# Performance work log

Hardware: AMD Instinct MI355X
Metric: run time of the kernel (lower is better)

Reference implementation:

```python
import jax, jax.numpy as jnp
import numpy as np

B, N, S, D, K = 8, 8192, 2048, 256, 3
MLP = [256, 128]
EPS = 1e-5


def setup_inputs() -> dict:
    key = jax.random.key(0)
    ks = jax.random.split(key, 12)
    inp = {
        "xyz1": jax.random.normal(ks[0], (B, N, 3), dtype=jnp.float32),
        "xyz2": jax.random.normal(ks[1], (B, S, 3), dtype=jnp.float32),
        "points1": jax.random.normal(ks[2], (B, N, D), dtype=jnp.float32),
        "points2": jax.random.normal(ks[3], (B, S, D), dtype=jnp.float32),
        # relation conv: Conv2d(4 -> 1, kernel 1x1) == linear over last dim
        "rel_w": jax.random.normal(ks[4], (4,), dtype=jnp.float32) * 0.5,
        "rel_b": jnp.zeros((), dtype=jnp.float32),
        # mlp layer 0: Conv1d(2D -> 256, k=1) + BN
        "W0": jax.random.normal(ks[5], (MLP[0], 2 * D), dtype=jnp.float32) * (1.0 / np.sqrt(2 * D)),
        "b0": jnp.zeros((MLP[0],), dtype=jnp.float32),
        "g0": jnp.ones((MLP[0],), dtype=jnp.float32),
        "be0": jnp.zeros((MLP[0],), dtype=jnp.float32),
        # mlp layer 1: Conv1d(256 -> 128, k=1) + BN
        "W1": jax.random.normal(ks[6], (MLP[1], MLP[0]), dtype=jnp.float32) * (1.0 / np.sqrt(MLP[0])),
        "b1": jnp.zeros((MLP[1],), dtype=jnp.float32),
        "g1": jnp.ones((MLP[1],), dtype=jnp.float32),
        "be1": jnp.zeros((MLP[1],), dtype=jnp.float32),
    }
    return inp


def _gather(points, idx):
    # points: [B,S,C], idx: [B,N,K] -> [B,N,K,C]
    return jax.vmap(lambda p, i: p[i])(points, idx)


def _bn_relu(x, gamma, beta):
    # training-mode BatchNorm1d over [B,N,C]: stats over (B,N), biased var
    mean = jnp.mean(x, axis=(0, 1))
    var = jnp.var(x, axis=(0, 1))
    xn = (x - mean) * jax.lax.rsqrt(var + EPS)
    return jax.nn.relu(xn * gamma + beta)


def reference(xyz1, xyz2, points1, points2, rel_w, rel_b,
              W0, b0, g0, be0, W1, b1, g1, be1):
    # pairwise squared distances [B,N,S]
    d = (jnp.sum(xyz1 ** 2, -1)[:, :, None]
         + jnp.sum(xyz2 ** 2, -1)[:, None, :]
         - 2.0 * jnp.einsum('bnc,bmc->bnm', xyz1, xyz2))
    neg_d, idx = jax.lax.top_k(-d, K)          # K smallest distances
    dists = -neg_d                              # [B,N,K]

    offset = xyz1[:, :, None, :] - _gather(xyz2, idx)        # [B,N,K,3]
    rel = jnp.concatenate([dists[..., None], offset], -1)    # [B,N,K,4]
    weight = jax.nn.sigmoid(rel @ rel_w + rel_b)              # [B,N,K]

    interp = jnp.mean(_gather(points2, idx) * weight[..., None], axis=2)  # [B,N,D]
    h = jnp.concatenate([points1, interp], axis=-1)           # [B,N,2D]

    h = _bn_relu(jnp.einsum('bnc,oc->bno', h, W0) + b0, g0, be0)
    h = _bn_relu(jnp.einsum('bnc,oc->bno', h, W1) + b1, g1, be1)
    return h  # [B,N,128]
```

## Files before the change

### kernel.cpp

```cpp
#include <hip/hip_runtime.h>
#include <stdint.h>
#include <stddef.h>

#define B_   8
#define N_   8192
#define S_   2048
#define D_   256
#define M_   (B_*N_)
#define C0_  256
#define C1_  128
#define K2D_ 512
#define TS8_ 8
#define SEG8_ (S_/TS8_)
#define SWP_ 264

typedef __attribute__((ext_vector_type(8))) short short8;
typedef __attribute__((ext_vector_type(4))) float f32x4;
typedef __attribute__((ext_vector_type(2))) float f32x2;

__device__ __forceinline__ short f2bf(float f) {
  unsigned u = __float_as_uint(f);
  u += 0x7fffu + ((u >> 16) & 1u);
  return (short)(u >> 16);
}
__device__ __forceinline__ float bf2f(short s) {
  return __uint_as_float(((unsigned)(unsigned short)s) << 16);
}

__device__ __forceinline__ void cp16(const void* g, void* l) {
  __builtin_amdgcn_global_load_lds(
      (__attribute__((address_space(1))) void*)(g),
      (__attribute__((address_space(3))) void*)(l), 16, 0, 0);
}

__device__ __forceinline__ double packdi(float d, int s) {
  return __longlong_as_double(__double_as_longlong((double)d) |
                              (unsigned long long)(unsigned)s);
}

#define PINS(v)                                                               \
  {                                                                           \
    const double v_ = (v);                                                    \
    double t_ = fmax(a0, v_); a0 = fmin(a0, v_);                              \
    double u_ = fmax(a1, t_); a1 = fmin(a1, t_);                              \
    a2 = fmin(a2, u_);                                                        \
  }

__global__ void convw_kernel(const float* __restrict__ W0,
                             const float* __restrict__ W1,
                             const float* __restrict__ xyz2,
                             short* __restrict__ W0b, short* __restrict__ W1b,
                             float* __restrict__ xyz2p, float* __restrict__ stats) {
  int i = blockIdx.x * 256 + threadIdx.x;
  if (blockIdx.x == 0) {
    stats[threadIdx.x] = 0.f;
    stats[256 + threadIdx.x] = 0.f;
    stats[512 + threadIdx.x] = 0.f;
  }
  if (i < C0_ * K2D_) W0b[i] = f2bf(W0[i]);
  if (i < C1_ * C0_)  W1b[i] = f2bf(W1[i]);
  if (i < B_ * S_) {
    const int b = i >> 11, s = i & (S_ - 1);
    float x = xyz2[(size_t)i * 3 + 0];
    float y = xyz2[(size_t)i * 3 + 1];
    float z = xyz2[(size_t)i * 3 + 2];
    float ss = __fadd_rn(__fadd_rn(__fmul_rn(x, x), __fmul_rn(y, y)), __fmul_rn(z, z));
    float* xw = xyz2p + (size_t)b * 4 * S_;
    xw[s] = x; xw[S_ + s] = y; xw[2 * S_ + s] = z; xw[3 * S_ + s] = ss;
  }
}

__global__ __launch_bounds__(512, 8)
void topk_interp_kernel(const float* __restrict__ xyz1, const float* __restrict__ xyz2p,
                        const float* __restrict__ relw, const float* __restrict__ relb,
                        const float* __restrict__ p2, short* __restrict__ hi) {
  __shared__ double cdp[TS8_][64][3];
  __shared__ int   sj[64][3];
  __shared__ float sw[64][3];
  const int tid  = threadIdx.x;
  const int lane = tid & 63;
  const int seg  = __builtin_amdgcn_readfirstlane(tid >> 6);
  const int b    = blockIdx.x >> 7;
  const int n    = (blockIdx.x & 127) * 64 + lane;

  const float* p = xyz1 + ((size_t)b * N_ + n) * 3;
  const float ax = p[0], ay = p[1], az = p[2];
  const float s1 = __fadd_rn(__fadd_rn(__fmul_rn(ax, ax), __fmul_rn(ay, ay)), __fmul_rn(az, az));

  const float* xw = xyz2p + (size_t)b * 4 * S_;
  const f32x2* XP = (const f32x2*)(xw)           + seg * (SEG8_ / 2);
  const f32x2* YP = (const f32x2*)(xw + S_)      + seg * (SEG8_ / 2);
  const f32x2* ZP = (const f32x2*)(xw + 2 * S_)  + seg * (SEG8_ / 2);
  const f32x2* WP = (const f32x2*)(xw + 3 * S_)  + seg * (SEG8_ / 2);

  double a0 = 1e300, a1 = 1e300, a2 = 1e300;
  const int sbeg = seg * SEG8_;
  {
    #pragma clang fp contract(off)
    #pragma unroll 4
    for (int pr = 0; pr < SEG8_ / 2; pr++) {
      f32x2 X = XP[pr], Y = YP[pr], Z = ZP[pr], W = WP[pr];
      f32x2 t1 = ax * X;
      f32x2 t2 = ay * Y;
      f32x2 t3 = az * Z;
      f32x2 dt = (t1 + t2) + t3;
      f32x2 e  = s1 + W;
      f32x2 m  = 2.0f * dt;
      f32x2 d  = e - m;
      const float dlo = fmaxf(d.x, 0.f), dhi = fmaxf(d.y, 0.f);
      const int s = sbeg + 2 * pr;
      const double p0 = packdi(dlo, s);
      const double p1 = packdi(dhi, s + 1);
      PINS(p0);
      PINS(p1);
    }
  }
  cdp[seg][lane][0] = a0; cdp[seg][lane][1] = a1; cdp[seg][lane][2] = a2;
  __syncthreads();

  if (tid < 64) {
    double a0 = 1e300, a1 = 1e300, a2 = 1e300;
    #pragma unroll
    for (int sg = 0; sg < TS8_; sg++) {
      #pragma unroll
      for (int k = 0; k < 3; k++) {
        const double v = cdp[sg][tid][k];
        PINS(v);
      }
    }
    const float w0r = relw[0], w1r = relw[1], w2r = relw[2], w3r = relw[3], br = relb[0];
    const double pk[3] = {a0, a1, a2};
    #pragma unroll
    for (int k = 0; k < 3; k++) {
      const int s = (int)(__double_as_longlong(pk[k]) & 2047ULL);
      const float dk = (float)pk[k];
      float ox = ax - xw[s], oy = ay - xw[S_ + s], oz = az - xw[2 * S_ + s];
      float t = dk * w0r + ox * w1r + oy * w2r + oz * w3r + br;
      float w = 1.0f / (1.0f + expf(-t));
      sj[tid][k] = s;
      sw[tid][k] = w * (1.0f / 3.0f);
    }
  }
  __syncthreads();

  {
    const int r = tid >> 3;
    const int c0 = (tid & 7) * 32;
    const size_t rowg = (size_t)b * N_ + (size_t)(blockIdx.x & 127) * 64 + r;
    const int j0 = sj[r][0], j1 = sj[r][1], j2 = sj[r][2];
    const float w0 = sw[r][0], w1 = sw[r][1], w2 = sw[r][2];
    const float* pb = p2 + (size_t)b * S_ * D_ + c0;
    const float* q0 = pb + (size_t)j0 * D_;
    const float* q1 = pb + (size_t)j1 * D_;
    const float* q2 = pb + (size_t)j2 * D_;
    short* dst = hi + rowg * D_ + c0;
    #pragma unroll
    for (int cc = 0; cc < 32; cc += 8) {
      const float4 a0v = *(const float4*)(q0 + cc), e0 = *(const float4*)(q0 + cc + 4);
      const float4 a1v = *(const float4*)(q1 + cc), e1 = *(const float4*)(q1 + cc + 4);
      const float4 a2v = *(const float4*)(q2 + cc), e2 = *(const float4*)(q2 + cc + 4);
      float fv[8];
      fv[0] = w0 * a0v.x + w1 * a1v.x + w2 * a2v.x;
      fv[1] = w0 * a0v.y + w1 * a1v.y + w2 * a2v.y;
      fv[2] = w0 * a0v.z + w1 * a1v.z + w2 * a2v.z;
      fv[3] = w0 * a0v.w + w1 * a1v.w + w2 * a2v.w;
      fv[4] = w0 * e0.x + w1 * e1.x + w2 * e2.x;
      fv[5] = w0 * e0.y + w1 * e1.y + w2 * e2.y;
      fv[6] = w0 * e0.z + w1 * e1.z + w2 * e2.z;
      fv[7] = w0 * e0.w + w1 * e1.w + w2 * e2.w;
      short8 o;
      #pragma unroll
      for (int e = 0; e < 8; e++) o[e] = f2bf(fv[e]);
      *(short8*)(dst + cc) = o;
    }
  }
}

__global__ __launch_bounds__(256, 2)
void gemm1_kernel(const float* __restrict__ p1, const short* __restrict__ hi,
                  const short* __restrict__ Bw, const float* __restrict__ bias,
                  short* __restrict__ Cb, float* __restrict__ stats) {
  __shared__ __align__(16) short sA[2][128 * 32];
  __shared__ __align__(16) short sB[2][256 * 32];
  const int tid = threadIdx.x;
  const int lane = tid & 63;
  const int wave = tid >> 6;
  const int wm = wave & 1;
  const int wn = wave >> 1;
  const size_t mbase = (size_t)(blockIdx.x & 7) * N_
                     + (size_t)(blockIdx.x >> 3) * 128;

  #define STAGE_A(K0, BUF)                                                    \
    if ((K0) < D_) {                                                          \
      _Pragma("unroll")                                                       \
      for (int t = 0; t < 2; t++) {                                           \
        const int c = tid * 2 + t;                                            \
        const int r = c >> 2; const int sc = (c & 3) * 8;                     \
        const float* src = p1 + (mbase + r) * D_ + (K0) + sc;                 \
        const float4 va = *(const float4*)src;                                \
        const float4 vb = *(const float4*)(src + 4);                          \
        short8 o;                                                             \
        o[0] = f2bf(va.x); o[1] = f2bf(va.y); o[2] = f2bf(va.z);              \
        o[3] = f2bf(va.w); o[4] = f2bf(vb.x); o[5] = f2bf(vb.y);              \
        o[6] = f2bf(vb.z); o[7] = f2bf(vb.w);                                 \
        *(short8*)&sA[BUF][r * 32 + sc] = o;                                  \
      }                                                                       \
    } else {                                                                  \
      _Pragma("unroll")                                                       \
      for (int t = 0; t < 2; t++) {                                           \
        const int ca = wave * 128 + t * 64 + lane;                            \
        cp16(hi + (mbase + (ca >> 2)) * D_ + ((K0) - D_) + (ca & 3) * 8,      \
             &sA[BUF][(wave * 128 + t * 64) * 8]);                            \
      }                                                                       \
    }

  #define STAGE_B(K0, BUF)                                                    \
    _Pragma("unroll")                                                         \
    for (int t = 0; t < 4; t++) {                                             \
      const int cb = wave * 256 + t * 64 + lane;                              \
      cp16(Bw + (size_t)(cb >> 2) * K2D_ + (K0) + (cb & 3) * 8,               \
           &sB[BUF][(wave * 256 + t * 64) * 8]);                              \
    }

  f32x4 acc[4][8] = {};
  STAGE_A(0, 0);
  STAGE_B(0, 0);

  const int mr = lane & 15;
  const int ks = (lane >> 4) * 8;

  for (int k0 = 0, it = 0; k0 < K2D_; k0 += 32, it++) {
    __syncthreads();
    const int kn = k0 + 32;
    if (kn < K2D_) {
      STAGE_A(kn, (it + 1) & 1);
      STAGE_B(kn, (it + 1) & 1);
    }

    short8 af[4], bfr[8];
    #pragma unroll
    for (int i = 0; i < 4; i++)
      af[i]  = *(const short8*)&sA[it & 1][(wm * 64 + i * 16 + mr) * 32 + ks];
    #pragma unroll
    for (int j = 0; j < 8; j++)
      bfr[j] = *(const short8*)&sB[it & 1][(wn * 128 + j * 16 + mr) * 32 + ks];
    #pragma unroll
    for (int i = 0; i < 4; i++)
      #pragma unroll
      for (int j = 0; j < 8; j++)
        acc[i][j] = __builtin_amdgcn_mfma_f32_16x16x32_bf16(af[i], bfr[j], acc[i][j], 0, 0, 0);
  }
  #undef STAGE_A
  #undef STAGE_B
  __syncthreads();

  const int cr = (lane >> 4) * 4;
  const int cc = lane & 15;
  float ps[8], ps2[8];
  #pragma unroll
  for (int j = 0; j < 8; j++) {
    const int col = wn * 128 + j * 16 + cc;
    const float bv = bias[col];
    float s = 0.f, s2 = 0.f;
    #pragma unroll
    for (int i = 0; i < 4; i++) {
      #pragma unroll
      for (int r = 0; r < 4; r++) {
        const float vv = acc[i][j][r];
        s += vv; s2 += vv * vv;
        const size_t row = mbase + wm * 64 + i * 16 + cr + r;
        Cb[row * C0_ + col] = f2bf(vv + bv);
      }
    }
    ps[j] = s; ps2[j] = s2;
  }
  #pragma unroll
  for (int j = 0; j < 8; j++) {
    ps[j]  += __shfl_xor(ps[j], 16);  ps[j]  += __shfl_xor(ps[j], 32);
    ps2[j] += __shfl_xor(ps2[j], 16); ps2[j] += __shfl_xor(ps2[j], 32);
  }
  float* sred = (float*)sA;
  if (wm == 1 && lane < 16) {
    #pragma unroll
    for (int j = 0; j < 8; j++) {
      const int c = wn * 128 + j * 16 + lane;
      sred[2 * c] = ps[j]; sred[2 * c + 1] = ps2[j];
    }
  }
  __syncthreads();
  if (wm == 0 && lane < 16) {
    #pragma unroll
    for (int j = 0; j < 8; j++) {
      const int c = wn * 128 + j * 16 + lane;
      atomicAdd(&stats[c],       ps[j]  + sred[2 * c]);
      atomicAdd(&stats[C0_ + c], ps2[j] + sred[2 * c + 1]);
    }
  }
}

__global__ __launch_bounds__(256, 2)
void gemm2_kernel(const short* __restrict__ A, const short* __restrict__ Bw,
                  const float* __restrict__ st1,
                  const float* __restrict__ b0, const float* __restrict__ g0,
                  const float* __restrict__ be0,
                  const float* __restrict__ bias,
                  short* __restrict__ Cb, float* __restrict__ stats) {
  __shared__ __align__(16) short sW[C1_ * SWP_];
  __shared__ float sred[3 * 256];
  __shared__ __align__(16) float sss[2 * C0_];
  const int tid = threadIdx.x;
  const int lane = tid & 63;
  const int wave = tid >> 6;
  const size_t mbase = (size_t)blockIdx.x * 128;

  {
    const float inv = 1.0f / (float)M_;
    const float m0 = st1[tid] * inv;
    const float var = st1[C0_ + tid] * inv - m0 * m0;
    const float mean = m0 + b0[tid];
    const float sc = g0[tid] * rsqrtf(var + 1e-5f);
    sss[tid] = sc;
    sss[C0_ + tid] = be0[tid] - mean * sc;
  }

  #pragma unroll
  for (int i = 0; i < 16; i++) {
    const int flat = i * 256 + tid;
    const int n = flat >> 5;
    const int kb = flat & 31;
    *(short8*)&sW[n * SWP_ + kb * 8] = *(const short8*)(Bw + (size_t)flat * 8);
  }
  __syncthreads();

  f32x4 acc[2][8] = {};
  const int mr = lane & 15;
  const int ksq = (lane >> 4) * 8;

  for (int k0 = 0; k0 < C0_; k0 += 32) {
    const int kk = k0 + ksq;
    float4 sc0 = *(const float4*)&sss[kk];
    float4 sc1 = *(const float4*)&sss[kk + 4];
    float4 sh0 = *(const float4*)&sss[C0_ + kk];
    float4 sh1 = *(const float4*)&sss[C0_ + kk + 4];
    const float sc[8] = {sc0.x, sc0.y, sc0.z, sc0.w, sc1.x, sc1.y, sc1.z, sc1.w};
    const float sh[8] = {sh0.x, sh0.y, sh0.z, sh0.w, sh1.x, sh1.y, sh1.z, sh1.w};
    short8 af[2];
    #pragma unroll
    for (int i = 0; i < 2; i++) {
      const size_t row = mbase + wave * 32 + i * 16 + mr;
      short8 av = *(const short8*)(A + row * C0_ + kk);
      short8 o;
      #pragma unroll
      for (int e = 0; e < 8; e++) {
        float f = bf2f(av[e]) * sc[e] + sh[e];
        o[e] = f2bf(f > 0.f ? f : 0.f);
      }
      af[i] = o;
    }
    short8 bf8[8];
    #pragma unroll
    for (int j = 0; j < 8; j++) bf8[j] = *(const short8*)&sW[(j * 16 + mr) * SWP_ + kk];
    #pragma unroll
    for (int i = 0; i < 2; i++)
      #pragma unroll
      for (int j = 0; j < 8; j++)
        acc[i][j] = __builtin_amdgcn_mfma_f32_16x16x32_bf16(af[i], bf8[j], acc[i][j], 0, 0, 0);
  }

  const int cr = (lane >> 4) * 4;
  const int cc = lane & 15;
  float ps[8], ps2[8];
  #pragma unroll
  for (int j = 0; j < 8; j++) {
    const int col = j * 16 + cc;
    const float bv = bias[col];
    float s = 0.f, s2 = 0.f;
    #pragma unroll
    for (int i = 0; i < 2; i++) {
      #pragma unroll
      for (int r = 0; r < 4; r++) {
        const float vv = acc[i][j][r];
        s += vv; s2 += vv * vv;
        const size_t row = mbase + wave * 32 + i * 16 + cr + r;
        Cb[row * C1_ + col] = f2bf(vv + bv);
      }
    }
    ps[j] = s; ps2[j] = s2;
  }
  #pragma unroll
  for (int j = 0; j < 8; j++) {
    ps[j]  += __shfl_xor(ps[j], 16);  ps[j]  += __shfl_xor(ps[j], 32);
    ps2[j] += __shfl_xor(ps2[j], 16); ps2[j] += __shfl_xor(ps2[j], 32);
  }
  if (wave > 0 && lane < 16) {
    #pragma unroll
    for (int j = 0; j < 8; j++) {
      const int c = j * 16 + lane;
      sred[(wave - 1) * 256 + c]       = ps[j];
      sred[(wave - 1) * 256 + 128 + c] = ps2[j];
    }
  }
  __syncthreads();
  if (wave == 0 && lane < 16) {
    #pragma unroll
    for (int j = 0; j < 8; j++) {
      const int c = j * 16 + lane;
      float s  = ps[j]  + sred[c]       + sred[256 + c]       + sred[512 + c];
      float s2 = ps2[j] + sred[128 + c] + sred[256 + 128 + c] + sred[512 + 128 + c];
      atomicAdd(&stats[c],       s);
      atomicAdd(&stats[C1_ + c], s2);
    }
  }
}

__global__ __launch_bounds__(256, 1)
void norm2_kernel(const short* __restrict__ a2, const float* __restrict__ st2,
                  const float* __restrict__ b1, const float* __restrict__ g1,
                  const float* __restrict__ be1, float* __restrict__ out) {
  __shared__ __align__(16) float sss[2 * C1_];
  const int tid = threadIdx.x;
  if (tid < C1_) {
    const float inv = 1.0f / (float)M_;
    const float m0 = st2[tid] * inv;
    const float var = st2[C1_ + tid] * inv - m0 * m0;
    const float mean = m0 + b1[tid];
    const float sc = g1[tid] * rsqrtf(var + 1e-5f);
    sss[tid] = sc;
    sss[C1_ + tid] = be1[tid] - mean * sc;
  }
  __syncthreads();
  const size_t t = (size_t)blockIdx.x * 256 + tid;
  const size_t base = t * 8;
  const int c = (int)(base & (C1_ - 1));
  short8 v8 = *(const short8*)(a2 + base);
  float vv[8];
  #pragma unroll
  for (int k = 0; k < 8; k++) {
    float v = bf2f(v8[k]) * sss[c + k] + sss[C1_ + c + k];
    vv[k] = v > 0.f ? v : 0.f;
  }
  *(float4*)(out + base)     = make_float4(vv[0], vv[1], vv[2], vv[3]);
  *(float4*)(out + base + 4) = make_float4(vv[4], vv[5], vv[6], vv[7]);
}

extern "C" void kernel_launch(void* const* d_in, const int* in_sizes, int n_in,
                              void* d_out, int out_size, void* d_ws, size_t ws_size,
                              hipStream_t stream) {
  const float* xyz1 = (const float*)d_in[0];
  const float* xyz2 = (const float*)d_in[1];
  const float* pts1 = (const float*)d_in[2];
  const float* pts2 = (const float*)d_in[3];
  const float* relw = (const float*)d_in[4];
  const float* relb = (const float*)d_in[5];
  const float* W0   = (const float*)d_in[6];
  const float* b0   = (const float*)d_in[7];
  const float* g0   = (const float*)d_in[8];
  const float* be0  = (const float*)d_in[9];
  const float* W1   = (const float*)d_in[10];
  const float* b1   = (const float*)d_in[11];
  const float* g1   = (const float*)d_in[12];
  const float* be1  = (const float*)d_in[13];

  char* ws = (char*)d_ws;
  constexpr size_t W0B_OFF = 0;
  constexpr size_t W1B_OFF = W0B_OFF + (size_t)C0_ * K2D_ * 2;
  constexpr size_t XW_OFF  = W1B_OFF + (size_t)C1_ * C0_ * 2;
  constexpr size_t HI_OFF  = XW_OFF + (size_t)B_ * 4 * S_ * 4;
  constexpr size_t A1_OFF  = HI_OFF + (size_t)M_ * D_ * 2;
  constexpr size_t A2_OFF  = A1_OFF + (size_t)M_ * C0_ * 2;
  constexpr size_t ST_OFF  = A2_OFF + (size_t)M_ * C1_ * 2;

  short* W0b   = (short*)(ws + W0B_OFF);
  short* W1b   = (short*)(ws + W1B_OFF);
  float* xyz2p = (float*)(ws + XW_OFF);
  short* hi    = (short*)(ws + HI_OFF);
  short* a1    = (short*)(ws + A1_OFF);
  short* a2    = (short*)(ws + A2_OFF);
  float* st    = (float*)(ws + ST_OFF);
  float* outp  = (float*)d_out;

  convw_kernel<<<512, 256, 0, stream>>>(W0, W1, xyz2, W0b, W1b, xyz2p, st);
  topk_interp_kernel<<<B_ * (N_ / 64), 512, 0, stream>>>(xyz1, xyz2p, relw, relb, pts2, hi);

  gemm1_kernel<<<M_ / 128, 256, 0, stream>>>(pts1, hi, W0b, b0, a1, st);
  gemm2_kernel<<<M_ / 128, 256, 0, stream>>>(a1, W1b, st, b0, g0, be0, b1, a2, st + 512);
  norm2_kernel<<<(size_t)M_ * C1_ / 8 / 256, 256, 0, stream>>>(a2, st + 512, b1, g1, be1, outp);
}
```

Measured before the change: 277.7 us.

## Widen top-k distance loads to float4 and read GEMM1 weights directly from global

In the top-k kernel, the distance loop now loads four candidate points per iteration with float4 vectors instead of two with float2, which halves the loop trip count and the number of load instructions. In gemm1, the shared-memory double buffer for the weight matrix is removed. Each wave now loads its B fragments straight from global memory (expected to hit L2) every k-step. This cuts LDS usage and the copies from LDS, which may raise occupancy, but every k-step now waits on global load latency that is no longer overlapped by prefetch.

```diff
diff --git a/kernel.cpp b/kernel.cpp
--- a/kernel.cpp
+++ b/kernel.cpp
@@ -88,31 +88,34 @@
   const float s1 = __fadd_rn(__fadd_rn(__fmul_rn(ax, ax), __fmul_rn(ay, ay)), __fmul_rn(az, az));
 
   const float* xw = xyz2p + (size_t)b * 4 * S_;
-  const f32x2* XP = (const f32x2*)(xw)           + seg * (SEG8_ / 2);
-  const f32x2* YP = (const f32x2*)(xw + S_)      + seg * (SEG8_ / 2);
-  const f32x2* ZP = (const f32x2*)(xw + 2 * S_)  + seg * (SEG8_ / 2);
-  const f32x2* WP = (const f32x2*)(xw + 3 * S_)  + seg * (SEG8_ / 2);
+  const f32x4* XP = (const f32x4*)(xw)           + seg * (SEG8_ / 4);
+  const f32x4* YP = (const f32x4*)(xw + S_)      + seg * (SEG8_ / 4);
+  const f32x4* ZP = (const f32x4*)(xw + 2 * S_)  + seg * (SEG8_ / 4);
+  const f32x4* WP = (const f32x4*)(xw + 3 * S_)  + seg * (SEG8_ / 4);
 
   double a0 = 1e300, a1 = 1e300, a2 = 1e300;
   const int sbeg = seg * SEG8_;
   {
     #pragma clang fp contract(off)
     #pragma unroll 4
-    for (int pr = 0; pr < SEG8_ / 2; pr++) {
-      f32x2 X = XP[pr], Y = YP[pr], Z = ZP[pr], W = WP[pr];
-      f32x2 t1 = ax * X;
-      f32x2 t2 = ay * Y;
-      f32x2 t3 = az * Z;
-      f32x2 dt = (t1 + t2) + t3;
-      f32x2 e  = s1 + W;
-      f32x2 m  = 2.0f * dt;
-      f32x2 d  = e - m;
-      const float dlo = fmaxf(d.x, 0.f), dhi = fmaxf(d.y, 0.f);
-      const int s = sbeg + 2 * pr;
-      const double p0 = packdi(dlo, s);
-      const double p1 = packdi(dhi, s + 1);
-      PINS(p0);
-      PINS(p1);
+    for (int pr = 0; pr < SEG8_ / 4; pr++) {
+      f32x4 X = XP[pr], Y = YP[pr], Z = ZP[pr], W = WP[pr];
+      f32x4 t1 = ax * X;
+      f32x4 t2 = ay * Y;
+      f32x4 t3 = az * Z;
+      f32x4 dt = (t1 + t2) + t3;
+      f32x4 e  = s1 + W;
+      f32x4 m  = 2.0f * dt;
+      f32x4 d  = e - m;
+      const int s = sbeg + 4 * pr;
+      const float d0c = fmaxf(d.x, 0.f);
+      const float d1c = fmaxf(d.y, 0.f);
+      const float d2c = fmaxf(d.z, 0.f);
+      const float d3c = fmaxf(d.w, 0.f);
+      PINS(packdi(d0c, s));
+      PINS(packdi(d1c, s + 1));
+      PINS(packdi(d2c, s + 2));
+      PINS(packdi(d3c, s + 3));
     }
   }
   cdp[seg][lane][0] = a0; cdp[seg][lane][1] = a1; cdp[seg][lane][2] = a2;
@@ -181,7 +184,6 @@
                   const short* __restrict__ Bw, const float* __restrict__ bias,
                   short* __restrict__ Cb, float* __restrict__ stats) {
   __shared__ __align__(16) short sA[2][128 * 32];
-  __shared__ __align__(16) short sB[2][256 * 32];
   const int tid = threadIdx.x;
   const int lane = tid & 63;
   const int wave = tid >> 6;
@@ -214,44 +216,32 @@
       }                                                                       \
     }
 
-  #define STAGE_B(K0, BUF)                                                    \
-    _Pragma("unroll")                                                         \
-    for (int t = 0; t < 4; t++) {                                             \
-      const int cb = wave * 256 + t * 64 + lane;                              \
-      cp16(Bw + (size_t)(cb >> 2) * K2D_ + (K0) + (cb & 3) * 8,               \
-           &sB[BUF][(wave * 256 + t * 64) * 8]);                              \
-    }
-
   f32x4 acc[4][8] = {};
   STAGE_A(0, 0);
-  STAGE_B(0, 0);
 
   const int mr = lane & 15;
   const int ks = (lane >> 4) * 8;
+  const short* Bbase = Bw + (size_t)(wn * 128 + mr) * K2D_ + ks;
 
   for (int k0 = 0, it = 0; k0 < K2D_; k0 += 32, it++) {
     __syncthreads();
     const int kn = k0 + 32;
-    if (kn < K2D_) {
-      STAGE_A(kn, (it + 1) & 1);
-      STAGE_B(kn, (it + 1) & 1);
-    }
+    if (kn < K2D_) STAGE_A(kn, (it + 1) & 1);
 
     short8 af[4], bfr[8];
+    #pragma unroll
+    for (int j = 0; j < 8; j++)
+      bfr[j] = *(const short8*)(Bbase + (size_t)j * 16 * K2D_ + k0);
     #pragma unroll
     for (int i = 0; i < 4; i++)
       af[i]  = *(const short8*)&sA[it & 1][(wm * 64 + i * 16 + mr) * 32 + ks];
     #pragma unroll
-    for (int j = 0; j < 8; j++)
-      bfr[j] = *(const short8*)&sB[it & 1][(wn * 128 + j * 16 + mr) * 32 + ks];
-    #pragma unroll
     for (int i = 0; i < 4; i++)
       #pragma unroll
       for (int j = 0; j < 8; j++)
         acc[i][j] = __builtin_amdgcn_mfma_f32_16x16x32_bf16(af[i], bfr[j], acc[i][j], 0, 0, 0);
   }
   #undef STAGE_A
-  #undef STAGE_B
   __syncthreads();
 
   const int cr = (lane >> 4) * 4;
```

Measured after the change: 288.6 us. 1.04x slower.
